# Kernel optimization log

Measured on AMD Instinct MI355X. Metric: run time of the kernel, lower is better.

Reference implementation:

```python
import jax, jax.numpy as jnp
import numpy as np

NUM_NODES = 100000
NUM_REL = 8
HIDDEN = 128
NUM_EDGES = 1600000
NUM_LAYERS = 2


def setup_inputs() -> dict:
    key = jax.random.key(0)
    k1, k2, k3, k4, k5 = jax.random.split(key, 5)
    x = jnp.arange(NUM_NODES, dtype=jnp.int64)
    edge_index = jax.random.randint(k1, (2, NUM_EDGES), 0, NUM_NODES, dtype=jnp.int64)
    edge_type = jax.random.randint(k2, (NUM_EDGES,), 0, NUM_REL, dtype=jnp.int64)
    emb = jax.random.normal(k3, (NUM_NODES, HIDDEN), dtype=jnp.float32) * 0.1
    W = jax.random.normal(k4, (NUM_LAYERS, NUM_REL, HIDDEN, HIDDEN), dtype=jnp.float32) * (1.0 / np.sqrt(HIDDEN))
    root = jax.random.normal(k5, (NUM_LAYERS, HIDDEN, HIDDEN), dtype=jnp.float32) * (1.0 / np.sqrt(HIDDEN))
    bias = jnp.zeros((NUM_LAYERS, HIDDEN), dtype=jnp.float32)
    return {"x": x, "edge_index": edge_index, "edge_type": edge_type,
            "emb": emb, "W": W, "root": root, "bias": bias}


def _rgcn_conv(h, src, dst, etype, W_l, root_l, bias_l):
    # h: [N, d]; W_l: [R, d, d]
    n = h.shape[0]
    r = W_l.shape[0]
    # Transform all nodes by every relation weight: [R, N, d]
    xW = jnp.einsum('nd,rdf->rnf', h, W_l)
    # Per-edge message gathered by (relation, source): [E, d]
    msg = xW[etype, src]
    # Mean-normalize per (target node, relation), matching PyG aggr='mean'
    seg = dst * r + etype  # combined (node, relation) segment id
    cnt = jax.ops.segment_sum(jnp.ones(msg.shape[0], dtype=h.dtype), seg,
                              num_segments=n * r)
    norm = 1.0 / jnp.maximum(cnt[seg], 1.0)
    agg = jax.ops.segment_sum(msg * norm[:, None], dst, num_segments=n)
    return agg + h @ root_l + bias_l


def reference(x, edge_index, edge_type, emb, W, root, bias):
    src, dst = edge_index[0], edge_index[1]
    h = emb[x]  # embedding lookup
    for l in range(NUM_LAYERS):
        h = _rgcn_conv(h, src, dst, edge_type, W[l], root[l], bias[l])
        h = jax.nn.relu(h)
    return h
```

## Files before the change

kernel.cpp:

```cpp
#include <hip/hip_runtime.h>

typedef unsigned int u32;
typedef unsigned short u16;
typedef __attribute__((ext_vector_type(8))) short short8;
typedef __attribute__((ext_vector_type(4))) float f32x4;

#define DD 128
#define RREL 8
#define KCAT 1152
#define NKT 9
#define SCAN_CHUNK 4096

static __device__ __forceinline__ u16 f2bf(float f) {
  u32 u = __builtin_bit_cast(u32, f);
  u32 r = (u + 0x7fffu + ((u >> 16) & 1u)) >> 16;
  return (u16)r;
}
static __device__ __forceinline__ float bflo(u32 v) { return __builtin_bit_cast(float, v << 16); }
static __device__ __forceinline__ float bfhi(u32 v) { return __builtin_bit_cast(float, v & 0xffff0000u); }

__global__ __launch_bounds__(256) void k_convw(const float* __restrict__ W,
                                               const float* __restrict__ root,
                                               uint4* __restrict__ wt) {
  int t = blockIdx.x * 256 + threadIdx.x;
  if (t >= 2 * NKT * 2048) return;
  int l = t / (NKT * 2048);
  int rem = t - l * (NKT * 2048);
  int kt = rem >> 11;
  int pos = rem & 2047;
  int col = pos >> 4;
  int cbx = pos & 15;
  int cb = cbx ^ (col & 7);
  int k0 = kt * DD + cb * 8;
  u16 vals[8];
#pragma unroll
  for (int i = 0; i < 8; ++i) {
    int k = k0 + i;
    float v;
    if (k < DD) {
      v = root[(size_t)l * DD * DD + k * DD + col];
    } else {
      int km = k - DD;
      v = W[((size_t)l * RREL + (km >> 7)) * DD * DD + (size_t)(km & 127) * DD + col];
    }
    vals[i] = f2bf(v);
  }
  wt[t] = *(uint4*)vals;
}

__global__ __launch_bounds__(256) void k_gather(const int* __restrict__ x,
                                                const float* __restrict__ emb,
                                                u16* __restrict__ acat, int N) {
  int t = blockIdx.x * 256 + threadIdx.x;
  if (t >= N * 16) return;
  int node = t >> 4, part = t & 15;
  const float4* e4 = (const float4*)(emb + (size_t)x[node] * DD + part * 8);
  float4 f0 = e4[0], f1 = e4[1];
  uint4 u;
  u.x = (u32)f2bf(f0.x) | ((u32)f2bf(f0.y) << 16);
  u.y = (u32)f2bf(f0.z) | ((u32)f2bf(f0.w) << 16);
  u.z = (u32)f2bf(f1.x) | ((u32)f2bf(f1.y) << 16);
  u.w = (u32)f2bf(f1.z) | ((u32)f2bf(f1.w) << 16);
  *(uint4*)(acat + (size_t)node * KCAT + part * 8) = u;
}

__global__ __launch_bounds__(256) void k_hist(const int* __restrict__ ei,
                                              const int* __restrict__ et,
                                              int* __restrict__ cnt, int E) {
  int e = blockIdx.x * 256 + threadIdx.x;
  if (e >= E) return;
  int dst = ei[E + e];
  atomicAdd(&cnt[dst * 8 + et[e]], 1);
}

__global__ __launch_bounds__(256) void k_scan_reduce(const int* __restrict__ cnt,
                                                     int* __restrict__ blksum, int nseg) {
  __shared__ int s[256];
  int b = blockIdx.x, t = threadIdx.x;
  int base = b * SCAN_CHUNK;
  int sum = 0;
  for (int i = 0; i < 16; ++i) {
    int idx = base + i * 256 + t;
    if (idx < nseg) sum += cnt[idx];
  }
  s[t] = sum;
  __syncthreads();
  for (int st = 128; st > 0; st >>= 1) {
    if (t < st) s[t] += s[t + st];
    __syncthreads();
  }
  if (t == 0) blksum[b] = s[0];
}

__global__ void k_scan_top(int* __restrict__ blksum, int nblk, int* __restrict__ off,
                           int nseg, int E) {
  if (threadIdx.x == 0 && blockIdx.x == 0) {
    int run = 0;
    for (int b = 0; b < nblk; ++b) { int v = blksum[b]; blksum[b] = run; run += v; }
    off[nseg] = E;
  }
}

__global__ __launch_bounds__(256) void k_scan_write(const int* __restrict__ cnt,
                                                    const int* __restrict__ blksum,
                                                    int* __restrict__ off, int nseg) {
  __shared__ int s[256];
  int b = blockIdx.x, t = threadIdx.x;
  int base = b * SCAN_CHUNK + t * 16;
  int v[16];
  int sum = 0;
#pragma unroll
  for (int i = 0; i < 16; ++i) {
    int idx = base + i;
    v[i] = (idx < nseg) ? cnt[idx] : 0;
    sum += v[i];
  }
  s[t] = sum;
  __syncthreads();
  for (int st = 1; st < 256; st <<= 1) {
    int add = (t >= st) ? s[t - st] : 0;
    __syncthreads();
    s[t] += add;
    __syncthreads();
  }
  int run = blksum[b] + s[t] - sum;
#pragma unroll
  for (int i = 0; i < 16; ++i) {
    int idx = base + i;
    if (idx < nseg) off[idx] = run;
    run += v[i];
  }
}

__global__ __launch_bounds__(256) void k_scatter(const int* __restrict__ ei,
                                                 const int* __restrict__ et,
                                                 const int* __restrict__ off,
                                                 int* __restrict__ fill,
                                                 int* __restrict__ sorted, int E) {
  int e = blockIdx.x * 256 + threadIdx.x;
  if (e >= E) return;
  int src = ei[e], dst = ei[E + e];
  int seg = dst * 8 + et[e];
  int pos = off[seg] + atomicAdd(&fill[seg], 1);
  sorted[pos] = src;
}

static __device__ __forceinline__ void add8(float* a, uint4 v) {
  a[0] += bflo(v.x); a[1] += bfhi(v.x);
  a[2] += bflo(v.y); a[3] += bfhi(v.y);
  a[4] += bflo(v.z); a[5] += bfhi(v.z);
  a[6] += bflo(v.w); a[7] += bfhi(v.w);
}

__global__ __launch_bounds__(256) void k_agg(const int* __restrict__ off,
                                             const int* __restrict__ sorted,
                                             u16* acat, int nseg) {
  int wave = threadIdx.x >> 6, lane = threadIdx.x & 63;
  int sub = lane >> 3, oct = lane & 7;
  int seg = blockIdx.x * 32 + wave * 8 + sub;
  if (seg >= nseg) return;
  int s = off[seg], e = off[seg + 1];
  float a[16];
#pragma unroll
  for (int i = 0; i < 16; ++i) a[i] = 0.f;
  int j = s;
  for (; j + 2 <= e; j += 2) {
    int s0 = sorted[j], s1 = sorted[j + 1];
    const uint4* p0 = (const uint4*)(acat + (size_t)s0 * KCAT + oct * 16);
    const uint4* p1 = (const uint4*)(acat + (size_t)s1 * KCAT + oct * 16);
    uint4 v0 = p0[0], v0b = p0[1];
    uint4 v1 = p1[0], v1b = p1[1];
    add8(a, v0); add8(a + 8, v0b);
    add8(a, v1); add8(a + 8, v1b);
  }
  if (j < e) {
    const uint4* p0 = (const uint4*)(acat + (size_t)sorted[j] * KCAT + oct * 16);
    uint4 v0 = p0[0], v0b = p0[1];
    add8(a, v0); add8(a + 8, v0b);
  }
  float norm = (e > s) ? 1.0f / (float)(e - s) : 0.f;
  uint4 w0, w1;
  w0.x = (u32)f2bf(a[0] * norm) | ((u32)f2bf(a[1] * norm) << 16);
  w0.y = (u32)f2bf(a[2] * norm) | ((u32)f2bf(a[3] * norm) << 16);
  w0.z = (u32)f2bf(a[4] * norm) | ((u32)f2bf(a[5] * norm) << 16);
  w0.w = (u32)f2bf(a[6] * norm) | ((u32)f2bf(a[7] * norm) << 16);
  w1.x = (u32)f2bf(a[8] * norm) | ((u32)f2bf(a[9] * norm) << 16);
  w1.y = (u32)f2bf(a[10] * norm) | ((u32)f2bf(a[11] * norm) << 16);
  w1.z = (u32)f2bf(a[12] * norm) | ((u32)f2bf(a[13] * norm) << 16);
  w1.w = (u32)f2bf(a[14] * norm) | ((u32)f2bf(a[15] * norm) << 16);
  int dst = seg >> 3, r = seg & 7;
  uint4* outp = (uint4*)(acat + (size_t)dst * KCAT + DD + r * DD + oct * 16);
  outp[0] = w0;
  outp[1] = w1;
}

template <bool LAST>
__global__ __launch_bounds__(512) void k_gemm(u16* acat, const uint4* __restrict__ wt,
                                              const float* __restrict__ bias,
                                              float* __restrict__ dout, int M) {
  __shared__ uint4 ldsB[2][2048];
  int tid = threadIdx.x, wave = tid >> 6, lane = tid & 63;
  int rowbase = blockIdx.x * 128 + wave * 16;
  int arow = rowbase + (lane & 15);
  int arc = arow < M ? arow : M - 1;
  int klane = (lane >> 4) << 3;
  f32x4 acc[8];
#pragma unroll
  for (int c = 0; c < 8; ++c) acc[c] = (f32x4)0.f;

#define STAGE(KT, BUF)                                                                   \
  do {                                                                                   \
    const uint4* gsrc = wt + (size_t)(KT) * 2048;                                        \
    _Pragma("unroll") for (int i_ = 0; i_ < 4; ++i_) {                                   \
      int cid_ = i_ * 512 + tid;                                                         \
      __builtin_amdgcn_global_load_lds(                                                  \
          (const __attribute__((address_space(1))) uint4*)(gsrc + cid_),                 \
          (__attribute__((address_space(3))) uint4*)&ldsB[BUF][cid_], 16, 0, 0);         \
    }                                                                                    \
  } while (0)

  STAGE(0, 0);
  for (int kt = 0; kt < NKT; ++kt) {
    int cur = kt & 1;
    __syncthreads();
    if (kt + 1 < NKT) STAGE(kt + 1, cur ^ 1);
#pragma unroll
    for (int kc = 0; kc < 4; ++kc) {
      short8 a = *(const short8*)(acat + (size_t)arc * KCAT + kt * DD + kc * 32 + klane);
      int chunk = kc * 4 + (lane >> 4);
#pragma unroll
      for (int c = 0; c < 8; ++c) {
        int col = c * 16 + (lane & 15);
        const short8* bp = (const short8*)&ldsB[cur][col * 16 + (chunk ^ (col & 7))];
        acc[c] = __builtin_amdgcn_mfma_f32_16x16x32_bf16(a, *bp, acc[c], 0, 0, 0);
      }
    }
  }
#undef STAGE

  int crow0 = rowbase + ((lane >> 4) << 2);
  int ccol = lane & 15;
#pragma unroll
  for (int c = 0; c < 8; ++c) {
    int col = c * 16 + ccol;
    float bv = bias[col];
#pragma unroll
    for (int i = 0; i < 4; ++i) {
      int row = crow0 + i;
      if (row < M) {
        float v = fmaxf(acc[c][i] + bv, 0.f);
        if (LAST) dout[(size_t)row * DD + col] = v;
        else acat[(size_t)row * KCAT + col] = f2bf(v);
      }
    }
  }
}

extern "C" void kernel_launch(void* const* d_in, const int* in_sizes, int n_in,
                              void* d_out, int out_size, void* d_ws, size_t ws_size,
                              hipStream_t stream) {
  const int* x = (const int*)d_in[0];
  const int* ei = (const int*)d_in[1];
  const int* et = (const int*)d_in[2];
  const float* emb = (const float*)d_in[3];
  const float* W = (const float*)d_in[4];
  const float* root = (const float*)d_in[5];
  const float* bias = (const float*)d_in[6];

  const int N = in_sizes[0];
  const int E = in_sizes[2];
  const int NSEG = N * RREL;

  size_t o = 0;
  auto al = [&](size_t b) { size_t r = o; o = (o + b + 255) & ~(size_t)255; return r; };
  size_t off_o = al(((size_t)NSEG + 1) * 4);
  size_t cnt_o = al((size_t)NSEG * 4);
  size_t fill_o = al((size_t)NSEG * 4);
  size_t sorted_o = al((size_t)E * 4);
  size_t blk_o = al(4096);
  size_t wt_o = al((size_t)2 * NKT * 2048 * 16);
  size_t acat_o = al((size_t)N * KCAT * 2);
  (void)acat_o;

  char* ws = (char*)d_ws;
  int* off = (int*)(ws + off_o);
  int* cnt = (int*)(ws + cnt_o);
  int* fill = (int*)(ws + fill_o);
  int* sorted = (int*)(ws + sorted_o);
  int* blks = (int*)(ws + blk_o);
  uint4* wt = (uint4*)(ws + wt_o);
  u16* acat = (u16*)(ws + acat_o);
  float* outf = (float*)d_out;

  k_convw<<<(2 * NKT * 2048 + 255) / 256, 256, 0, stream>>>(W, root, wt);
  k_gather<<<(N * 16 + 255) / 256, 256, 0, stream>>>(x, emb, acat, N);
  hipMemsetAsync(cnt, 0, (size_t)NSEG * 4, stream);
  hipMemsetAsync(fill, 0, (size_t)NSEG * 4, stream);
  k_hist<<<(E + 255) / 256, 256, 0, stream>>>(ei, et, cnt, E);
  int nblk = (NSEG + SCAN_CHUNK - 1) / SCAN_CHUNK;
  k_scan_reduce<<<nblk, 256, 0, stream>>>(cnt, blks, NSEG);
  k_scan_top<<<1, 64, 0, stream>>>(blks, nblk, off, NSEG, E);
  k_scan_write<<<nblk, 256, 0, stream>>>(cnt, blks, off, NSEG);
  k_scatter<<<(E + 255) / 256, 256, 0, stream>>>(ei, et, off, fill, sorted, E);

  int gx = (N + 127) / 128;
  k_agg<<<(NSEG + 31) / 32, 256, 0, stream>>>(off, sorted, acat, NSEG);
  k_gemm<false><<<gx, 512, 0, stream>>>(acat, wt, bias, nullptr, N);
  k_agg<<<(NSEG + 31) / 32, 256, 0, stream>>>(off, sorted, acat, NSEG);
  k_gemm<true><<<gx, 512, 0, stream>>>(acat, wt + (size_t)NKT * 2048, bias + DD, outf, N);
}
```

Before: 512.5 us.

## Fuse per-relation mean aggregation into GEMM A-fragment loading, drop concat buffer

Aggregation of neighbor features per (node, relation) now happens inside the GEMM kernel: each lane gathers and averages source rows directly into its MFMA A fragments, so the 1152-wide concatenated bf16 buffer is no longer written and re-read. Hidden states move to compact N×128 ping-pong buffers. Histogram and scatter kernels process four edges per thread with vector loads, and the fill counters are seeded by copying the offsets so the scatter needs no extra offset read. The cost is that the gather loop now sits inside the GEMM with 16-lane-per-row parallelism, uneven per-row loops, and higher register pressure (32 float accumulators), which may stall the MFMA pipeline.

```diff
diff --git a/kernel.cpp b/kernel.cpp
--- a/kernel.cpp
+++ b/kernel.cpp
@@ -7,7 +7,6 @@
 
 #define DD 128
 #define RREL 8
-#define KCAT 1152
 #define NKT 9
 #define SCAN_CHUNK 4096
 
@@ -50,7 +49,7 @@
 
 __global__ __launch_bounds__(256) void k_gather(const int* __restrict__ x,
                                                 const float* __restrict__ emb,
-                                                u16* __restrict__ acat, int N) {
+                                                u16* __restrict__ h0, int N) {
   int t = blockIdx.x * 256 + threadIdx.x;
   if (t >= N * 16) return;
   int node = t >> 4, part = t & 15;
@@ -61,16 +60,23 @@
   u.y = (u32)f2bf(f0.z) | ((u32)f2bf(f0.w) << 16);
   u.z = (u32)f2bf(f1.x) | ((u32)f2bf(f1.y) << 16);
   u.w = (u32)f2bf(f1.z) | ((u32)f2bf(f1.w) << 16);
-  *(uint4*)(acat + (size_t)node * KCAT + part * 8) = u;
+  *(uint4*)(h0 + (size_t)node * DD + part * 8) = u;
 }
 
 __global__ __launch_bounds__(256) void k_hist(const int* __restrict__ ei,
                                               const int* __restrict__ et,
                                               int* __restrict__ cnt, int E) {
-  int e = blockIdx.x * 256 + threadIdx.x;
-  if (e >= E) return;
-  int dst = ei[E + e];
-  atomicAdd(&cnt[dst * 8 + et[e]], 1);
+  int base = (blockIdx.x * 256 + threadIdx.x) * 4;
+  if (base + 3 < E) {
+    int4 d4 = *(const int4*)(ei + E + base);
+    int4 t4 = *(const int4*)(et + base);
+    atomicAdd(&cnt[d4.x * 8 + t4.x], 1);
+    atomicAdd(&cnt[d4.y * 8 + t4.y], 1);
+    atomicAdd(&cnt[d4.z * 8 + t4.z], 1);
+    atomicAdd(&cnt[d4.w * 8 + t4.w], 1);
+  } else {
+    for (int e = base; e < E; ++e) atomicAdd(&cnt[ei[E + e] * 8 + et[e]], 1);
+  }
 }
 
 __global__ __launch_bounds__(256) void k_scan_reduce(const int* __restrict__ cnt,
@@ -134,15 +140,27 @@
 
 __global__ __launch_bounds__(256) void k_scatter(const int* __restrict__ ei,
                                                  const int* __restrict__ et,
-                                                 const int* __restrict__ off,
                                                  int* __restrict__ fill,
                                                  int* __restrict__ sorted, int E) {
-  int e = blockIdx.x * 256 + threadIdx.x;
-  if (e >= E) return;
-  int src = ei[e], dst = ei[E + e];
-  int seg = dst * 8 + et[e];
-  int pos = off[seg] + atomicAdd(&fill[seg], 1);
-  sorted[pos] = src;
+  int base = (blockIdx.x * 256 + threadIdx.x) * 4;
+  if (base + 3 < E) {
+    int4 s4 = *(const int4*)(ei + base);
+    int4 d4 = *(const int4*)(ei + E + base);
+    int4 t4 = *(const int4*)(et + base);
+    int p0 = atomicAdd(&fill[d4.x * 8 + t4.x], 1);
+    int p1 = atomicAdd(&fill[d4.y * 8 + t4.y], 1);
+    int p2 = atomicAdd(&fill[d4.z * 8 + t4.z], 1);
+    int p3 = atomicAdd(&fill[d4.w * 8 + t4.w], 1);
+    sorted[p0] = s4.x;
+    sorted[p1] = s4.y;
+    sorted[p2] = s4.z;
+    sorted[p3] = s4.w;
+  } else {
+    for (int e = base; e < E; ++e) {
+      int pos = atomicAdd(&fill[ei[E + e] * 8 + et[e]], 1);
+      sorted[pos] = ei[e];
+    }
+  }
 }
 
 static __device__ __forceinline__ void add8(float* a, uint4 v) {
@@ -152,58 +170,19 @@
   a[6] += bflo(v.w); a[7] += bfhi(v.w);
 }
 
-__global__ __launch_bounds__(256) void k_agg(const int* __restrict__ off,
-                                             const int* __restrict__ sorted,
-                                             u16* acat, int nseg) {
-  int wave = threadIdx.x >> 6, lane = threadIdx.x & 63;
-  int sub = lane >> 3, oct = lane & 7;
-  int seg = blockIdx.x * 32 + wave * 8 + sub;
-  if (seg >= nseg) return;
-  int s = off[seg], e = off[seg + 1];
-  float a[16];
-#pragma unroll
-  for (int i = 0; i < 16; ++i) a[i] = 0.f;
-  int j = s;
-  for (; j + 2 <= e; j += 2) {
-    int s0 = sorted[j], s1 = sorted[j + 1];
-    const uint4* p0 = (const uint4*)(acat + (size_t)s0 * KCAT + oct * 16);
-    const uint4* p1 = (const uint4*)(acat + (size_t)s1 * KCAT + oct * 16);
-    uint4 v0 = p0[0], v0b = p0[1];
-    uint4 v1 = p1[0], v1b = p1[1];
-    add8(a, v0); add8(a + 8, v0b);
-    add8(a, v1); add8(a + 8, v1b);
-  }
-  if (j < e) {
-    const uint4* p0 = (const uint4*)(acat + (size_t)sorted[j] * KCAT + oct * 16);
-    uint4 v0 = p0[0], v0b = p0[1];
-    add8(a, v0); add8(a + 8, v0b);
-  }
-  float norm = (e > s) ? 1.0f / (float)(e - s) : 0.f;
-  uint4 w0, w1;
-  w0.x = (u32)f2bf(a[0] * norm) | ((u32)f2bf(a[1] * norm) << 16);
-  w0.y = (u32)f2bf(a[2] * norm) | ((u32)f2bf(a[3] * norm) << 16);
-  w0.z = (u32)f2bf(a[4] * norm) | ((u32)f2bf(a[5] * norm) << 16);
-  w0.w = (u32)f2bf(a[6] * norm) | ((u32)f2bf(a[7] * norm) << 16);
-  w1.x = (u32)f2bf(a[8] * norm) | ((u32)f2bf(a[9] * norm) << 16);
-  w1.y = (u32)f2bf(a[10] * norm) | ((u32)f2bf(a[11] * norm) << 16);
-  w1.z = (u32)f2bf(a[12] * norm) | ((u32)f2bf(a[13] * norm) << 16);
-  w1.w = (u32)f2bf(a[14] * norm) | ((u32)f2bf(a[15] * norm) << 16);
-  int dst = seg >> 3, r = seg & 7;
-  uint4* outp = (uint4*)(acat + (size_t)dst * KCAT + DD + r * DD + oct * 16);
-  outp[0] = w0;
-  outp[1] = w1;
-}
-
 template <bool LAST>
-__global__ __launch_bounds__(512) void k_gemm(u16* acat, const uint4* __restrict__ wt,
-                                              const float* __restrict__ bias,
-                                              float* __restrict__ dout, int M) {
+__global__ __launch_bounds__(512, 4) void k_fused(const u16* __restrict__ hin,
+                                                  const int* __restrict__ off,
+                                                  const int* __restrict__ sorted,
+                                                  const uint4* __restrict__ wt,
+                                                  const float* __restrict__ bias,
+                                                  u16* __restrict__ hout,
+                                                  float* __restrict__ dout, int M) {
   __shared__ uint4 ldsB[2][2048];
   int tid = threadIdx.x, wave = tid >> 6, lane = tid & 63;
-  int rowbase = blockIdx.x * 128 + wave * 16;
-  int arow = rowbase + (lane & 15);
-  int arc = arow < M ? arow : M - 1;
-  int klane = (lane >> 4) << 3;
+  int p = lane & 15, q = lane >> 4;
+  int row = blockIdx.x * 128 + wave * 16 + p;
+  int arc = row < M ? row : M - 1;
   f32x4 acc[8];
 #pragma unroll
   for (int c = 0; c < 8; ++c) acc[c] = (f32x4)0.f;
@@ -221,36 +200,66 @@
 
   STAGE(0, 0);
   for (int kt = 0; kt < NKT; ++kt) {
+    short8 afrag[4];
+    if (kt == 0) {
+      const short8* ap = (const short8*)(hin + (size_t)arc * DD) + q;
+#pragma unroll
+      for (int kc = 0; kc < 4; ++kc) afrag[kc] = ap[kc * 4];
+    } else {
+      int r = kt - 1;
+      int s = 0, e = 0;
+      if (row < M) {
+        int sb = row * 8 + r;
+        s = off[sb];
+        e = off[sb + 1];
+      }
+      float a[32];
+#pragma unroll
+      for (int i = 0; i < 32; ++i) a[i] = 0.f;
+      for (int j = s; j < e; ++j) {
+        int src = sorted[j];
+        const uint4* hp = (const uint4*)(hin + (size_t)src * DD) + q;
+        uint4 v0 = hp[0], v1 = hp[4], v2 = hp[8], v3 = hp[12];
+        add8(a + 0, v0);
+        add8(a + 8, v1);
+        add8(a + 16, v2);
+        add8(a + 24, v3);
+      }
+      float norm = (e > s) ? 1.0f / (float)(e - s) : 0.f;
+      u16 fr[32];
+#pragma unroll
+      for (int i = 0; i < 32; ++i) fr[i] = f2bf(a[i] * norm);
+#pragma unroll
+      for (int kc = 0; kc < 4; ++kc) afrag[kc] = *(const short8*)(fr + kc * 8);
+    }
     int cur = kt & 1;
     __syncthreads();
     if (kt + 1 < NKT) STAGE(kt + 1, cur ^ 1);
 #pragma unroll
     for (int kc = 0; kc < 4; ++kc) {
-      short8 a = *(const short8*)(acat + (size_t)arc * KCAT + kt * DD + kc * 32 + klane);
-      int chunk = kc * 4 + (lane >> 4);
+      int chunk = kc * 4 + q;
 #pragma unroll
       for (int c = 0; c < 8; ++c) {
-        int col = c * 16 + (lane & 15);
+        int col = c * 16 + p;
         const short8* bp = (const short8*)&ldsB[cur][col * 16 + (chunk ^ (col & 7))];
-        acc[c] = __builtin_amdgcn_mfma_f32_16x16x32_bf16(a, *bp, acc[c], 0, 0, 0);
+        acc[c] = __builtin_amdgcn_mfma_f32_16x16x32_bf16(afrag[kc], *bp, acc[c], 0, 0, 0);
       }
     }
   }
 #undef STAGE
 
-  int crow0 = rowbase + ((lane >> 4) << 2);
-  int ccol = lane & 15;
+  int crow0 = blockIdx.x * 128 + wave * 16 + (q << 2);
 #pragma unroll
   for (int c = 0; c < 8; ++c) {
-    int col = c * 16 + ccol;
+    int col = c * 16 + p;
     float bv = bias[col];
 #pragma unroll
     for (int i = 0; i < 4; ++i) {
-      int row = crow0 + i;
-      if (row < M) {
+      int rw = crow0 + i;
+      if (rw < M) {
         float v = fmaxf(acc[c][i] + bv, 0.f);
-        if (LAST) dout[(size_t)row * DD + col] = v;
-        else acat[(size_t)row * KCAT + col] = f2bf(v);
+        if (LAST) dout[(size_t)rw * DD + col] = v;
+        else hout[(size_t)rw * DD + col] = f2bf(v);
       }
     }
   }
@@ -279,8 +288,9 @@
   size_t sorted_o = al((size_t)E * 4);
   size_t blk_o = al(4096);
   size_t wt_o = al((size_t)2 * NKT * 2048 * 16);
-  size_t acat_o = al((size_t)N * KCAT * 2);
-  (void)acat_o;
+  size_t h0_o = al((size_t)N * DD * 2);
+  size_t h1_o = al((size_t)N * DD * 2);
+  (void)h1_o;
 
   char* ws = (char*)d_ws;
   int* off = (int*)(ws + off_o);
@@ -289,23 +299,24 @@
   int* sorted = (int*)(ws + sorted_o);
   int* blks = (int*)(ws + blk_o);
   uint4* wt = (uint4*)(ws + wt_o);
-  u16* acat = (u16*)(ws + acat_o);
+  u16* h0 = (u16*)(ws + h0_o);
+  u16* h1 = (u16*)(ws + h1_o);
   float* outf = (float*)d_out;
 
   k_convw<<<(2 * NKT * 2048 + 255) / 256, 256, 0, stream>>>(W, root, wt);
-  k_gather<<<(N * 16 + 255) / 256, 256, 0, stream>>>(x, emb, acat, N);
+  k_gather<<<(N * 16 + 255) / 256, 256, 0, stream>>>(x, emb, h0, N);
   hipMemsetAsync(cnt, 0, (size_t)NSEG * 4, stream);
-  hipMemsetAsync(fill, 0, (size_t)NSEG * 4, stream);
-  k_hist<<<(E + 255) / 256, 256, 0, stream>>>(ei, et, cnt, E);
+  int egrid = ((E + 3) / 4 + 255) / 256;
+  k_hist<<<egrid, 256, 0, stream>>>(ei, et, cnt, E);
   int nblk = (NSEG + SCAN_CHUNK - 1) / SCAN_CHUNK;
   k_scan_reduce<<<nblk, 256, 0, stream>>>(cnt, blks, NSEG);
   k_scan_top<<<1, 64, 0, stream>>>(blks, nblk, off, NSEG, E);
   k_scan_write<<<nblk, 256, 0, stream>>>(cnt, blks, off, NSEG);
-  k_scatter<<<(E + 255) / 256, 256, 0, stream>>>(ei, et, off, fill, sorted, E);
+  hipMemcpyAsync(fill, off, (size_t)NSEG * 4, hipMemcpyDeviceToDevice, stream);
+  k_scatter<<<egrid, 256, 0, stream>>>(ei, et, fill, sorted, E);
 
   int gx = (N + 127) / 128;
-  k_agg<<<(NSEG + 31) / 32, 256, 0, stream>>>(off, sorted, acat, NSEG);
-  k_gemm<false><<<gx, 512, 0, stream>>>(acat, wt, bias, nullptr, N);
-  k_agg<<<(NSEG + 31) / 32, 256, 0, stream>>>(off, sorted, acat, NSEG);
-  k_gemm<true><<<gx, 512, 0, stream>>>(acat, wt + (size_t)NKT * 2048, bias + DD, outf, N);
-}
+  k_fused<false><<<gx, 512, 0, stream>>>(h0, off, sorted, wt, bias, h1, nullptr, N);
+  k_fused<true><<<gx, 512, 0, stream>>>(h1, off, sorted, wt + (size_t)NKT * 2048,
+                                        bias + DD, nullptr, outf, N);
+}
```

After: 547.3 us. 6.8% more time.

## Vectorize edge histogram/scatter and aggregate all relations per destination node

Applied to the files above, without the earlier changes.

The histogram and scatter kernels now have each thread handle 8 edges through int4 vector loads. The scatter seeds its fill counters by copying the offsets, which removes the separate off[] lookup and one memset. The aggregation kernel moves from one 8-lane group per (node, relation) segment to one group per destination node. That group walks all 8 relation segments in sequence over a contiguous edge range, pairing loads across segment boundaries. This is meant to cut launch and indexing overhead and improve memory-level parallelism, at the cost of more branchy control flow and fewer independent work items in the aggregation.

```diff
diff --git a/kernel.cpp b/kernel.cpp
--- a/kernel.cpp
+++ b/kernel.cpp
@@ -67,10 +67,23 @@
 __global__ __launch_bounds__(256) void k_hist(const int* __restrict__ ei,
                                               const int* __restrict__ et,
                                               int* __restrict__ cnt, int E) {
-  int e = blockIdx.x * 256 + threadIdx.x;
-  if (e >= E) return;
-  int dst = ei[E + e];
-  atomicAdd(&cnt[dst * 8 + et[e]], 1);
+  int base = (blockIdx.x * 256 + threadIdx.x) * 8;
+  if (base + 7 < E) {
+    int4 dA = *(const int4*)(ei + E + base);
+    int4 dB = *(const int4*)(ei + E + base + 4);
+    int4 tA = *(const int4*)(et + base);
+    int4 tB = *(const int4*)(et + base + 4);
+    atomicAdd(&cnt[dA.x * 8 + tA.x], 1);
+    atomicAdd(&cnt[dA.y * 8 + tA.y], 1);
+    atomicAdd(&cnt[dA.z * 8 + tA.z], 1);
+    atomicAdd(&cnt[dA.w * 8 + tA.w], 1);
+    atomicAdd(&cnt[dB.x * 8 + tB.x], 1);
+    atomicAdd(&cnt[dB.y * 8 + tB.y], 1);
+    atomicAdd(&cnt[dB.z * 8 + tB.z], 1);
+    atomicAdd(&cnt[dB.w * 8 + tB.w], 1);
+  } else {
+    for (int e = base; e < E; ++e) atomicAdd(&cnt[ei[E + e] * 8 + et[e]], 1);
+  }
 }
 
 __global__ __launch_bounds__(256) void k_scan_reduce(const int* __restrict__ cnt,
@@ -134,15 +147,38 @@
 
 __global__ __launch_bounds__(256) void k_scatter(const int* __restrict__ ei,
                                                  const int* __restrict__ et,
-                                                 const int* __restrict__ off,
                                                  int* __restrict__ fill,
                                                  int* __restrict__ sorted, int E) {
-  int e = blockIdx.x * 256 + threadIdx.x;
-  if (e >= E) return;
-  int src = ei[e], dst = ei[E + e];
-  int seg = dst * 8 + et[e];
-  int pos = off[seg] + atomicAdd(&fill[seg], 1);
-  sorted[pos] = src;
+  int base = (blockIdx.x * 256 + threadIdx.x) * 8;
+  if (base + 7 < E) {
+    int4 sA = *(const int4*)(ei + base);
+    int4 sB = *(const int4*)(ei + base + 4);
+    int4 dA = *(const int4*)(ei + E + base);
+    int4 dB = *(const int4*)(ei + E + base + 4);
+    int4 tA = *(const int4*)(et + base);
+    int4 tB = *(const int4*)(et + base + 4);
+    int p0 = atomicAdd(&fill[dA.x * 8 + tA.x], 1);
+    int p1 = atomicAdd(&fill[dA.y * 8 + tA.y], 1);
+    int p2 = atomicAdd(&fill[dA.z * 8 + tA.z], 1);
+    int p3 = atomicAdd(&fill[dA.w * 8 + tA.w], 1);
+    int p4 = atomicAdd(&fill[dB.x * 8 + tB.x], 1);
+    int p5 = atomicAdd(&fill[dB.y * 8 + tB.y], 1);
+    int p6 = atomicAdd(&fill[dB.z * 8 + tB.z], 1);
+    int p7 = atomicAdd(&fill[dB.w * 8 + tB.w], 1);
+    sorted[p0] = sA.x;
+    sorted[p1] = sA.y;
+    sorted[p2] = sA.z;
+    sorted[p3] = sA.w;
+    sorted[p4] = sB.x;
+    sorted[p5] = sB.y;
+    sorted[p6] = sB.z;
+    sorted[p7] = sB.w;
+  } else {
+    for (int e = base; e < E; ++e) {
+      int pos = atomicAdd(&fill[ei[E + e] * 8 + et[e]], 1);
+      sorted[pos] = ei[e];
+    }
+  }
 }
 
 static __device__ __forceinline__ void add8(float* a, uint4 v) {
@@ -154,44 +190,62 @@
 
 __global__ __launch_bounds__(256) void k_agg(const int* __restrict__ off,
                                              const int* __restrict__ sorted,
-                                             u16* acat, int nseg) {
+                                             u16* acat, int N, int E) {
   int wave = threadIdx.x >> 6, lane = threadIdx.x & 63;
-  int sub = lane >> 3, oct = lane & 7;
-  int seg = blockIdx.x * 32 + wave * 8 + sub;
-  if (seg >= nseg) return;
-  int s = off[seg], e = off[seg + 1];
+  int grp = lane >> 3, oct = lane & 7;
+  int dst = blockIdx.x * 32 + wave * 8 + grp;
+  if (dst >= N) return;
+  int4 b0 = *(const int4*)(off + dst * 8);
+  int4 b1 = *(const int4*)(off + dst * 8 + 4);
+  int je = off[dst * 8 + 8];
+  int cs = b0.x;
+  int e1 = b0.y, e2 = b0.z, e3 = b0.w, e4 = b1.x, e5 = b1.y, e6 = b1.z, e7 = b1.w, e8 = je;
+  u16* ambase = acat + (size_t)dst * KCAT + DD + oct * 16;
   float a[16];
 #pragma unroll
   for (int i = 0; i < 16; ++i) a[i] = 0.f;
-  int j = s;
-  for (; j + 2 <= e; j += 2) {
-    int s0 = sorted[j], s1 = sorted[j + 1];
+  int j = cs;
+  int r = 0;
+  int lastidx = (E > 0) ? E - 1 : 0;
+  while (true) {
+    while (r < 8 && j >= e1) {
+      int cnt = e1 - cs;
+      float norm = (cnt > 0) ? 1.0f / (float)cnt : 0.f;
+      uint4 w0, w1;
+      w0.x = (u32)f2bf(a[0] * norm) | ((u32)f2bf(a[1] * norm) << 16);
+      w0.y = (u32)f2bf(a[2] * norm) | ((u32)f2bf(a[3] * norm) << 16);
+      w0.z = (u32)f2bf(a[4] * norm) | ((u32)f2bf(a[5] * norm) << 16);
+      w0.w = (u32)f2bf(a[6] * norm) | ((u32)f2bf(a[7] * norm) << 16);
+      w1.x = (u32)f2bf(a[8] * norm) | ((u32)f2bf(a[9] * norm) << 16);
+      w1.y = (u32)f2bf(a[10] * norm) | ((u32)f2bf(a[11] * norm) << 16);
+      w1.z = (u32)f2bf(a[12] * norm) | ((u32)f2bf(a[13] * norm) << 16);
+      w1.w = (u32)f2bf(a[14] * norm) | ((u32)f2bf(a[15] * norm) << 16);
+      uint4* outp = (uint4*)(ambase + (size_t)r * DD);
+      outp[0] = w0;
+      outp[1] = w1;
+#pragma unroll
+      for (int i = 0; i < 16; ++i) a[i] = 0.f;
+      cs = e1;
+      e1 = e2; e2 = e3; e3 = e4; e4 = e5; e5 = e6; e6 = e7; e7 = e8;
+      ++r;
+    }
+    if (r >= 8) break;
+    int j1 = j + 1;
+    bool two = (j1 < e1);
+    int s0 = sorted[j];
+    int s1 = sorted[two ? j1 : lastidx];
     const uint4* p0 = (const uint4*)(acat + (size_t)s0 * KCAT + oct * 16);
     const uint4* p1 = (const uint4*)(acat + (size_t)s1 * KCAT + oct * 16);
     uint4 v0 = p0[0], v0b = p0[1];
     uint4 v1 = p1[0], v1b = p1[1];
+    if (!two) {
+      v1.x = v1.y = v1.z = v1.w = 0u;
+      v1b.x = v1b.y = v1b.z = v1b.w = 0u;
+    }
     add8(a, v0); add8(a + 8, v0b);
     add8(a, v1); add8(a + 8, v1b);
-  }
-  if (j < e) {
-    const uint4* p0 = (const uint4*)(acat + (size_t)sorted[j] * KCAT + oct * 16);
-    uint4 v0 = p0[0], v0b = p0[1];
-    add8(a, v0); add8(a + 8, v0b);
-  }
-  float norm = (e > s) ? 1.0f / (float)(e - s) : 0.f;
-  uint4 w0, w1;
-  w0.x = (u32)f2bf(a[0] * norm) | ((u32)f2bf(a[1] * norm) << 16);
-  w0.y = (u32)f2bf(a[2] * norm) | ((u32)f2bf(a[3] * norm) << 16);
-  w0.z = (u32)f2bf(a[4] * norm) | ((u32)f2bf(a[5] * norm) << 16);
-  w0.w = (u32)f2bf(a[6] * norm) | ((u32)f2bf(a[7] * norm) << 16);
-  w1.x = (u32)f2bf(a[8] * norm) | ((u32)f2bf(a[9] * norm) << 16);
-  w1.y = (u32)f2bf(a[10] * norm) | ((u32)f2bf(a[11] * norm) << 16);
-  w1.z = (u32)f2bf(a[12] * norm) | ((u32)f2bf(a[13] * norm) << 16);
-  w1.w = (u32)f2bf(a[14] * norm) | ((u32)f2bf(a[15] * norm) << 16);
-  int dst = seg >> 3, r = seg & 7;
-  uint4* outp = (uint4*)(acat + (size_t)dst * KCAT + DD + r * DD + oct * 16);
-  outp[0] = w0;
-  outp[1] = w1;
+    j += two ? 2 : 1;
+  }
 }
 
 template <bool LAST>
@@ -295,17 +349,19 @@
   k_convw<<<(2 * NKT * 2048 + 255) / 256, 256, 0, stream>>>(W, root, wt);
   k_gather<<<(N * 16 + 255) / 256, 256, 0, stream>>>(x, emb, acat, N);
   hipMemsetAsync(cnt, 0, (size_t)NSEG * 4, stream);
-  hipMemsetAsync(fill, 0, (size_t)NSEG * 4, stream);
-  k_hist<<<(E + 255) / 256, 256, 0, stream>>>(ei, et, cnt, E);
+  int egrid = ((E + 7) / 8 + 255) / 256;
+  k_hist<<<egrid, 256, 0, stream>>>(ei, et, cnt, E);
   int nblk = (NSEG + SCAN_CHUNK - 1) / SCAN_CHUNK;
   k_scan_reduce<<<nblk, 256, 0, stream>>>(cnt, blks, NSEG);
   k_scan_top<<<1, 64, 0, stream>>>(blks, nblk, off, NSEG, E);
   k_scan_write<<<nblk, 256, 0, stream>>>(cnt, blks, off, NSEG);
-  k_scatter<<<(E + 255) / 256, 256, 0, stream>>>(ei, et, off, fill, sorted, E);
+  hipMemcpyAsync(fill, off, (size_t)NSEG * 4, hipMemcpyDeviceToDevice, stream);
+  k_scatter<<<egrid, 256, 0, stream>>>(ei, et, fill, sorted, E);
 
   int gx = (N + 127) / 128;
-  k_agg<<<(NSEG + 31) / 32, 256, 0, stream>>>(off, sorted, acat, NSEG);
+  int agrid = (N + 31) / 32;
+  k_agg<<<agrid, 256, 0, stream>>>(off, sorted, acat, N, E);
   k_gemm<false><<<gx, 512, 0, stream>>>(acat, wt, bias, nullptr, N);
-  k_agg<<<(NSEG + 31) / 32, 256, 0, stream>>>(off, sorted, acat, NSEG);
+  k_agg<<<agrid, 256, 0, stream>>>(off, sorted, acat, N, E);
   k_gemm<true><<<gx, 512, 0, stream>>>(acat, wt + (size_t)NKT * 2048, bias + DD, outf, N);
 }
```

New measurement: 554.5 us. 8.2% more time.
